# Optimization experiments

Measured on AMD Instinct MI355X. Metric: run time of the kernel, lower is better.

## Reference

```python
import jax, jax.numpy as jnp
import numpy as np

N_ROI = 116; G = 128; DEG = 32
N = G * N_ROI          # 14848 nodes
E = G * N_ROI * DEG    # 475136 edges
HID = 64; HEADS = 4; HC = HEADS * HID  # 256
EDIM = 5; EMB = 16; NG = 8; OUT = 2
NEG = 0.01      # nn.LeakyReLU default slope
NEG_ATT = 0.2   # GATv2 internal negative_slope
EPS = 1e-5


def leaky(x, s=NEG):
    return jnp.where(x >= 0, x, s * x)


def seg_softmax(logits, seg, n):
    # numerically stable softmax over edges grouped by target node
    m = jax.ops.segment_max(logits, seg, num_segments=n)
    m = jnp.where(jnp.isfinite(m), m, 0.0)
    ex = jnp.exp(logits - m[seg])
    s = jax.ops.segment_sum(ex, seg, num_segments=n)
    return ex / (s[seg] + 1e-16)


def _xav(k, shape):
    return jax.random.normal(k, shape, jnp.float32) * np.sqrt(2.0 / sum(shape)).astype(np.float32)


def setup_inputs() -> dict:
    key = jax.random.key(0)
    ks = jax.random.split(key, 40)
    x = jax.random.normal(ks[0], (N, N_ROI), jnp.float32)
    off = (jnp.arange(G, dtype=jnp.int32) * N_ROI)[:, None]
    src = (jax.random.randint(ks[1], (G, N_ROI * DEG), 0, N_ROI, jnp.int32) + off).reshape(-1)
    dst = (jax.random.randint(ks[2], (G, N_ROI * DEG), 0, N_ROI, jnp.int32) + off).reshape(-1)
    edge_index = jnp.stack([src, dst])  # [2, E], block-diagonal per graph
    edge_attr = jax.random.normal(ks[3], (E, EDIM), jnp.float32)
    grp = np.repeat(np.arange(NG, dtype=np.int32), [15] * 7 + [11])  # partition of 116 ROIs
    node_group = jnp.tile(jnp.asarray(grp), G)
    batch = jnp.repeat(jnp.arange(G, dtype=jnp.int32), N_ROI)
    p = {
        'group_emb': _xav(ks[4], (NG, EMB)),
        'W_embed': _xav(ks[5], (N_ROI + EMB, HID)), 'b_embed': jnp.zeros((HID,), jnp.float32),
        'We_enc': _xav(ks[6], (EDIM, HID)), 'be_enc': jnp.zeros((HID,), jnp.float32),
        'W1': _xav(ks[7], (HID, HID)), 'b1': jnp.zeros((HID,), jnp.float32),
        'W2': _xav(ks[8], (HID, HID)), 'b2': jnp.zeros((HID,), jnp.float32),
        'ln_g': jnp.ones((HID,), jnp.float32), 'ln_b': jnp.zeros((HID,), jnp.float32),
        'l0_Wl': _xav(ks[9], (HID, HC)), 'l0_Wr': _xav(ks[10], (HID, HC)),
        'l0_We': _xav(ks[11], (EDIM, HC)), 'l0_att': _xav(ks[12], (HEADS, HID)),
        'l0_b': jnp.zeros((HC,), jnp.float32),
        'l0_bn_g': jnp.ones((HC,), jnp.float32), 'l0_bn_b': jnp.zeros((HC,), jnp.float32),
        'l1_Wl': _xav(ks[13], (HC, HC)), 'l1_Wr': _xav(ks[14], (HC, HC)),
        'l1_We': _xav(ks[15], (EDIM, HC)), 'l1_att': _xav(ks[16], (HEADS, HID)),
        'l1_b': jnp.zeros((HC,), jnp.float32),
        'l1_bn_g': jnp.ones((HC,), jnp.float32), 'l1_bn_b': jnp.zeros((HC,), jnp.float32),
        'fc2_W': _xav(ks[17], (HC, OUT)), 'fc2_b': jnp.zeros((OUT,), jnp.float32),
    }
    return dict(x=x, edge_index=edge_index, edge_attr=edge_attr, batch=batch, node_group=node_group, **p)


def _gat_layer(h, src, dst, edge_attr, Wl, Wr, We, att, b, bn_g, bn_b):
    n = h.shape[0]
    xl = (h @ Wl).reshape(n, HEADS, HID)
    xr = (h @ Wr).reshape(n, HEADS, HID)
    e = (edge_attr @ We).reshape(-1, HEADS, HID)
    xls = xl[src]                                   # [E,H,C]
    z = leaky(xls + xr[dst] + e, NEG_ATT)
    logits = jnp.einsum('ehc,hc->eh', z, att)       # GATv2 attention scores
    alpha = seg_softmax(logits, dst, n)             # softmax over incoming edges per node
    out = jax.ops.segment_sum(xls * alpha[:, :, None], dst, num_segments=n)
    out = out.reshape(n, HC) + b
    mu = out.mean(0); var = ((out - mu) ** 2).mean(0)  # BatchNorm (batch stats)
    out = (out - mu) / jnp.sqrt(var + EPS) * bn_g + bn_b
    return leaky(out)


def reference(x, edge_index, edge_attr, batch, node_group, group_emb, W_embed, b_embed,
              We_enc, be_enc, W1, b1, W2, b2, ln_g, ln_b,
              l0_Wl, l0_Wr, l0_We, l0_att, l0_b, l0_bn_g, l0_bn_b,
              l1_Wl, l1_Wr, l1_We, l1_att, l1_b, l1_bn_g, l1_bn_b, fc2_W, fc2_b):
    src, dst = edge_index[0], edge_index[1]
    # BrainEncodeEmbed: group embedding concat + projection
    h = jnp.concatenate([x, group_emb[node_group]], axis=-1)   # [N, 132]
    h = leaky(h @ W_embed + b_embed)                            # [N, HID]
    eemb = leaky(edge_attr @ We_enc + be_enc)                   # [E, HID]
    # GINEConv: sum_j ReLU(x_j + e_ij), eps=0, then MLP
    msg = jax.nn.relu(h[src] + eemb)
    h = h + jax.ops.segment_sum(msg, dst, num_segments=N)
    h = leaky(h @ W1 + b1) @ W2 + b2
    h = leaky(h)
    mu = h.mean(-1, keepdims=True)
    v = ((h - mu) ** 2).mean(-1, keepdims=True)
    h = (h - mu) / jnp.sqrt(v + EPS) * ln_g + ln_b              # LayerNorm
    # stacked GATv2 blocks
    h = _gat_layer(h, src, dst, edge_attr, l0_Wl, l0_Wr, l0_We, l0_att, l0_b, l0_bn_g, l0_bn_b)
    h = _gat_layer(h, src, dst, edge_attr, l1_Wl, l1_Wr, l1_We, l1_att, l1_b, l1_bn_g, l1_bn_b)
    # global mean pool + classifier
    cnt = jax.ops.segment_sum(jnp.ones((h.shape[0],), h.dtype), batch, num_segments=G)
    pooled = jax.ops.segment_sum(h, batch, num_segments=G) / cnt[:, None]
    return pooled @ fc2_W + fc2_b
```

## Files before the change

### kernel.cpp

```cpp
#include <hip/hip_runtime.h>
#include <hip/hip_bf16.h>

#define NN     14848
#define NE     475136
#define NROI   116
#define NGRAPH 128
#define EPG    3712
#define HID    64
#define HC     256
#define NEG    0.01f
#define NEGA   0.2f
#define EPB    2304
#define XPAD   65

typedef __attribute__((ext_vector_type(8))) short short8;
typedef __attribute__((ext_vector_type(4))) float floatx4;

__device__ __forceinline__ float leaky(float x, float s) { return fmaxf(x, s * x); }

__device__ __forceinline__ short f2bf(float f) {
    unsigned u = __float_as_uint(f);
    unsigned r = (u + 0x7fffu + ((u >> 16) & 1u)) >> 16;
    return (short)r;
}

__global__ __launch_bounds__(256) void k_embed(
    const float* __restrict__ x, const int* __restrict__ ng,
    const float* __restrict__ gemb, const float* __restrict__ W,
    const float* __restrict__ b, float* __restrict__ h0)
{
    const int w = threadIdx.x >> 6, c = threadIdx.x & 63;
    const int n = blockIdx.x * 4 + w;
    __shared__ float in[4][132];
    for (int k = c; k < NROI; k += 64) in[w][k] = x[n * NROI + k];
    if (c < 16) in[w][NROI + c] = gemb[ng[n] * 16 + c];
    __syncthreads();
    float acc = b[c];
    #pragma unroll 4
    for (int k = 0; k < 132; k++) acc = fmaf(in[w][k], W[k * 64 + c], acc);
    h0[n * 64 + c] = leaky(acc, NEG);
}

__global__ __launch_bounds__(256) void k_csr(
    const int* __restrict__ src, const int* __restrict__ dst,
    const float* __restrict__ ea,
    int* __restrict__ row_start, int* __restrict__ row_cnt,
    int* __restrict__ ssd, float* __restrict__ ea_s)
{
    const int g = blockIdx.x, tid = threadIdx.x;
    const int e0 = g * EPG, nb = g * NROI;
    __shared__ int cnt[NROI], start[NROI], cur[NROI];
    if (tid < NROI) cnt[tid] = 0;
    __syncthreads();
    for (int i = tid; i < EPG; i += 256) atomicAdd(&cnt[dst[e0 + i] - nb], 1);
    __syncthreads();
    if (tid == 0) {
        int s = 0;
        for (int r = 0; r < NROI; r++) { start[r] = s; s += cnt[r]; }
    }
    __syncthreads();
    if (tid < NROI) {
        row_start[nb + tid] = e0 + start[tid];
        row_cnt[nb + tid] = cnt[tid];
        cur[tid] = start[tid];
    }
    __syncthreads();
    for (int i = tid; i < EPG; i += 256) {
        const int e = e0 + i, dl = dst[e] - nb;
        const int pos = atomicAdd(&cur[dl], 1);
        const int gi = e0 + pos;
        ssd[gi] = (src[e] - nb) | (dl << 16);
        const float4 q = make_float4(ea[e * 5], ea[e * 5 + 1], ea[e * 5 + 2], ea[e * 5 + 3]);
        *(float4*)&ea_s[(size_t)gi * 8] = q;
        ea_s[(size_t)gi * 8 + 4] = ea[e * 5 + 4];
    }
}

__global__ __launch_bounds__(64) void k_prep_w(
    const float* __restrict__ Wl0, const float* __restrict__ Wr0,
    const float* __restrict__ Wl1, const float* __restrict__ Wr1,
    short* __restrict__ Wt0, short* __restrict__ Wt1)
{
    if (blockIdx.x < 512) {
        const int n = blockIdx.x;
        for (int k = threadIdx.x; k < 64; k += 64) {
            const float v = (n < 256) ? Wl0[k * 256 + n] : Wr0[k * 256 + (n - 256)];
            Wt0[(size_t)n * 64 + k] = f2bf(v);
        }
    } else {
        const int n = blockIdx.x - 512;
        for (int k = threadIdx.x; k < 256; k += 64) {
            const float v = (n < 256) ? Wl1[k * 256 + n] : Wr1[k * 256 + (n - 256)];
            Wt1[(size_t)n * 256 + k] = f2bf(v);
        }
    }
}

__global__ __launch_bounds__(256) void k_gine_mlp_ln(
    const float* __restrict__ h0, const int* __restrict__ row_start,
    const int* __restrict__ row_cnt, const int* __restrict__ ssd,
    const float* __restrict__ ea_s,
    const float* __restrict__ We, const float* __restrict__ be,
    const float* __restrict__ W1, const float* __restrict__ b1,
    const float* __restrict__ W2, const float* __restrict__ b2,
    const float* __restrict__ lg_, const float* __restrict__ lb_,
    short* __restrict__ hn)
{
    const int tid = threadIdx.x, w = tid >> 6, lane = tid & 63;
    const int row = blockIdx.x * 4 + w;
    const int nb = (row / NROI) * NROI;
    const int st = row_start[row], cnt = row_cnt[row];
    const float w0 = We[lane], w1 = We[64 + lane], w2 = We[128 + lane],
                w3 = We[192 + lane], w4 = We[256 + lane];
    const float bec = be[lane];
    float g0 = 0.f, g1 = 0.f;
    int j = 0;
    for (; j + 2 <= cnt; j += 2) {
        const int ia = st + j, ib = st + j + 1;
        const int sa = nb + (ssd[ia] & 0xffff), sb = nb + (ssd[ib] & 0xffff);
        const float4 qa = *(const float4*)&ea_s[(size_t)ia * 8];
        const float qa4 = ea_s[(size_t)ia * 8 + 4];
        const float4 qb = *(const float4*)&ea_s[(size_t)ib * 8];
        const float qb4 = ea_s[(size_t)ib * 8 + 4];
        float ea_ = bec, eb_ = bec;
        ea_ = fmaf(qa.x, w0, ea_); eb_ = fmaf(qb.x, w0, eb_);
        ea_ = fmaf(qa.y, w1, ea_); eb_ = fmaf(qb.y, w1, eb_);
        ea_ = fmaf(qa.z, w2, ea_); eb_ = fmaf(qb.z, w2, eb_);
        ea_ = fmaf(qa.w, w3, ea_); eb_ = fmaf(qb.w, w3, eb_);
        ea_ = fmaf(qa4, w4, ea_);  eb_ = fmaf(qb4, w4, eb_);
        g0 += fmaxf(h0[sa * 64 + lane] + leaky(ea_, NEG), 0.f);
        g1 += fmaxf(h0[sb * 64 + lane] + leaky(eb_, NEG), 0.f);
    }
    for (; j < cnt; j++) {
        const int idx = st + j;
        const int s = nb + (ssd[idx] & 0xffff);
        const float4 q = *(const float4*)&ea_s[(size_t)idx * 8];
        const float q4 = ea_s[(size_t)idx * 8 + 4];
        float em = bec;
        em = fmaf(q.x, w0, em); em = fmaf(q.y, w1, em); em = fmaf(q.z, w2, em);
        em = fmaf(q.w, w3, em); em = fmaf(q4, w4, em);
        g0 += fmaxf(h0[s * 64 + lane] + leaky(em, NEG), 0.f);
    }
    const float aggv = g0 + g1;
    __shared__ float v[4][64], t[4][64];
    v[w][lane] = h0[row * 64 + lane] + aggv;
    __syncthreads();
    float a = b1[lane];
    #pragma unroll 8
    for (int k = 0; k < 64; k++) a = fmaf(v[w][k], W1[k * 64 + lane], a);
    t[w][lane] = leaky(a, NEG);
    __syncthreads();
    float o = b2[lane];
    #pragma unroll 8
    for (int k = 0; k < 64; k++) o = fmaf(t[w][k], W2[k * 64 + lane], o);
    o = leaky(o, NEG);
    float s = o;
    #pragma unroll
    for (int off = 32; off; off >>= 1) s += __shfl_xor(s, off);
    const float mu = s * (1.f / 64.f);
    const float d = o - mu;
    float s2 = d * d;
    #pragma unroll
    for (int off = 32; off; off >>= 1) s2 += __shfl_xor(s2, off);
    hn[row * 64 + lane] = f2bf(d * rsqrtf(s2 * (1.f / 64.f) + 1e-5f) * lg_[lane] + lb_[lane]);
}

__global__ __launch_bounds__(256) void k_bn_bf16(
    const float* __restrict__ V, const float* __restrict__ stats,
    const float* __restrict__ bg, const float* __restrict__ bb,
    short* __restrict__ Hb)
{
    const int n = blockIdx.x, c = threadIdx.x;
    const float inv_n = 1.f / (float)NN;
    const float mu = stats[c] * inv_n;
    float var = stats[256 + c] * inv_n - mu * mu;
    var = fmaxf(var, 0.f);
    const float rsg = rsqrtf(var + 1e-5f) * bg[c];
    const float o = (V[(size_t)n * HC + c] - mu) * rsg + bb[c];
    Hb[(size_t)n * HC + c] = f2bf(leaky(o, NEG));
}

template <int D>
__global__ __launch_bounds__(256) void k_gemm(
    const short* __restrict__ A, const short* __restrict__ Wt,
    float* __restrict__ X, float* __restrict__ Y)
{
    const int m0 = blockIdx.x * 16;
    const int w = threadIdx.x >> 6, lane = threadIdx.x & 63;
    const int n0 = w * 128;
    const int r = lane & 15, q = lane >> 4;
    floatx4 acc[8];
    #pragma unroll
    for (int t = 0; t < 8; t++) acc[t] = (floatx4){0.f, 0.f, 0.f, 0.f};
    const short* Arow = A + (size_t)(m0 + r) * D + q * 8;
    const short* Brow = Wt + (size_t)(n0 + r) * D + q * 8;
    #pragma unroll
    for (int k0 = 0; k0 < D; k0 += 32) {
        const short8 a = *(const short8*)(Arow + k0);
        #pragma unroll
        for (int t = 0; t < 8; t++) {
            const short8 b = *(const short8*)(Brow + (size_t)t * 16 * D + k0);
            acc[t] = __builtin_amdgcn_mfma_f32_16x16x32_bf16(a, b, acc[t], 0, 0, 0);
        }
    }
    #pragma unroll
    for (int t = 0; t < 8; t++) {
        const int ncol = n0 + t * 16 + r;
        #pragma unroll
        for (int g2 = 0; g2 < 4; g2++) {
            const int row = m0 + q * 4 + g2;
            if (ncol < 256) X[(size_t)row * HC + ncol] = acc[t][g2];
            else            Y[(size_t)row * HC + (ncol - 256)] = acc[t][g2];
        }
    }
}

__global__ __launch_bounds__(256, 4) void k_gat(
    const int* __restrict__ row_start, const int* __restrict__ row_cnt,
    const int* __restrict__ ssd, const float* __restrict__ ea_s,
    const float* __restrict__ We, const float* __restrict__ att,
    const float* __restrict__ bias,
    const float* __restrict__ X, const float* __restrict__ Y,
    float* __restrict__ V, float* __restrict__ stats)
{
    const int g = blockIdx.x >> 3;
    const int h = (blockIdx.x >> 1) & 3;
    const int half = blockIdx.x & 1;
    const int tid = threadIdx.x, w = tid >> 6, lane = tid & 63;
    const int nb = g * NROI, e0 = g * EPG, hc = h * 64;
    const int r0 = half * 58, r1 = r0 + 58;
    const int es = row_start[nb + r0];
    const int ee = (r1 < NROI) ? row_start[nb + r1] : e0 + EPG;

    __shared__ float Xs[NROI * XPAD];
    __shared__ float lg[EPB];
    __shared__ float inv_s[58];

    for (int r = w; r < NROI; r += 4)
        Xs[r * XPAD + lane] = X[(size_t)(nb + r) * HC + hc + lane];
    __syncthreads();

    const int ne = ee - es;
    for (int i = tid; i < ne; i += 256) {
        const int e = es + i;
        const int sd = ssd[e];
        const int sl = sd & 0xffff, dl = sd >> 16;
        const float4 q = *(const float4*)&ea_s[(size_t)e * 8];
        const float q4 = ea_s[(size_t)e * 8 + 4];
        const float* yrow = &Y[(size_t)(nb + dl) * HC + hc];
        const int xb = sl * XPAD;
        float lacc = 0.f;
        #pragma unroll 8
        for (int c = 0; c < 64; c++) {
            float ep = q.x * We[0 * HC + hc + c];
            ep = fmaf(q.y, We[1 * HC + hc + c], ep);
            ep = fmaf(q.z, We[2 * HC + hc + c], ep);
            ep = fmaf(q.w, We[3 * HC + hc + c], ep);
            ep = fmaf(q4, We[4 * HC + hc + c], ep);
            const float z = Xs[xb + c] + yrow[c] + ep;
            lacc = fmaf(att[hc + c], leaky(z, NEGA), lacc);
        }
        lg[i] = lacc;
    }
    __syncthreads();

    for (int r = r0 + w; r < r1; r += 4) {
        const int stl = row_start[nb + r] - es;
        const int cnt = row_cnt[nb + r];
        float m = -INFINITY;
        for (int j = lane; j < cnt; j += 64) m = fmaxf(m, lg[stl + j]);
        #pragma unroll
        for (int off = 32; off; off >>= 1) m = fmaxf(m, __shfl_xor(m, off));
        float s = 0.f;
        for (int j = lane; j < cnt; j += 64) {
            const float e_ = __expf(lg[stl + j] - m);
            lg[stl + j] = e_;
            s += e_;
        }
        #pragma unroll
        for (int off = 32; off; off >>= 1) s += __shfl_xor(s, off);
        if (lane == 0) inv_s[r - r0] = 1.f / (s + 1e-16f);
    }
    __syncthreads();

    float ps = 0.f, ps2 = 0.f;
    const float bb = bias[hc + lane];
    for (int r = r0 + w; r < r1; r += 4) {
        const int st = row_start[nb + r];
        const int cnt = row_cnt[nb + r];
        const int stl = st - es;
        float a0 = 0.f, a1 = 0.f, a2 = 0.f, a3 = 0.f;
        int j = 0;
        for (; j + 4 <= cnt; j += 4) {
            const int s0 = ssd[st + j] & 0xffff, s1 = ssd[st + j + 1] & 0xffff,
                      s2 = ssd[st + j + 2] & 0xffff, s3 = ssd[st + j + 3] & 0xffff;
            a0 = fmaf(Xs[s0 * XPAD + lane], lg[stl + j], a0);
            a1 = fmaf(Xs[s1 * XPAD + lane], lg[stl + j + 1], a1);
            a2 = fmaf(Xs[s2 * XPAD + lane], lg[stl + j + 2], a2);
            a3 = fmaf(Xs[s3 * XPAD + lane], lg[stl + j + 3], a3);
        }
        for (; j < cnt; j++)
            a0 = fmaf(Xs[(ssd[st + j] & 0xffff) * XPAD + lane], lg[stl + j], a0);
        const float vv = ((a0 + a1) + (a2 + a3)) * inv_s[r - r0] + bb;
        V[(size_t)(nb + r) * HC + hc + lane] = vv;
        ps += vv;
        ps2 += vv * vv;
    }
    __syncthreads();
    lg[tid] = ps;
    lg[256 + tid] = ps2;
    __syncthreads();
    if (tid < 64) {
        float s1 = 0.f, s2 = 0.f;
        #pragma unroll
        for (int w2 = 0; w2 < 4; w2++) {
            s1 += lg[w2 * 64 + tid];
            s2 += lg[256 + w2 * 64 + tid];
        }
        atomicAdd(&stats[hc + tid], s1);
        atomicAdd(&stats[256 + hc + tid], s2);
    }
}

__global__ __launch_bounds__(256) void k_pool_fc(
    const float* __restrict__ V, const float* __restrict__ stats,
    const float* __restrict__ bg, const float* __restrict__ bb,
    const float* __restrict__ fW, const float* __restrict__ fb,
    float* __restrict__ out)
{
    const int g = blockIdx.x, c = threadIdx.x;
    const float inv_n = 1.f / (float)NN;
    const float mu = stats[c] * inv_n;
    float var = stats[256 + c] * inv_n - mu * mu;
    var = fmaxf(var, 0.f);
    const float rsg = rsqrtf(var + 1e-5f) * bg[c];
    const float bbc = bb[c];
    float s = 0.f;
    for (int r = 0; r < NROI; r++) {
        const float vv = (V[(size_t)(g * NROI + r) * HC + c] - mu) * rsg + bbc;
        s += leaky(vv, NEG);
    }
    s *= (1.f / (float)NROI);
    __shared__ float red[256];
    for (int o = 0; o < 2; o++) {
        red[c] = s * fW[c * 2 + o];
        __syncthreads();
        for (int off = 128; off; off >>= 1) {
            if (c < off) red[c] += red[c + off];
            __syncthreads();
        }
        if (c == 0) out[g * 2 + o] = red[0] + fb[o];
        __syncthreads();
    }
}

extern "C" void kernel_launch(void* const* d_in, const int* in_sizes, int n_in,
                              void* d_out, int out_size, void* d_ws, size_t ws_size,
                              hipStream_t stream) {
    const float* x         = (const float*)d_in[0];
    const int*   edge_idx  = (const int*)d_in[1];
    const float* edge_attr = (const float*)d_in[2];
    const int*   node_grp  = (const int*)d_in[4];
    const float* group_emb = (const float*)d_in[5];
    const float* W_embed   = (const float*)d_in[6];
    const float* b_embed   = (const float*)d_in[7];
    const float* We_enc    = (const float*)d_in[8];
    const float* be_enc    = (const float*)d_in[9];
    const float* W1        = (const float*)d_in[10];
    const float* b1        = (const float*)d_in[11];
    const float* W2        = (const float*)d_in[12];
    const float* b2        = (const float*)d_in[13];
    const float* ln_g      = (const float*)d_in[14];
    const float* ln_b      = (const float*)d_in[15];
    const float* l0_Wl     = (const float*)d_in[16];
    const float* l0_Wr     = (const float*)d_in[17];
    const float* l0_We     = (const float*)d_in[18];
    const float* l0_att    = (const float*)d_in[19];
    const float* l0_b      = (const float*)d_in[20];
    const float* l0_bn_g   = (const float*)d_in[21];
    const float* l0_bn_b   = (const float*)d_in[22];
    const float* l1_Wl     = (const float*)d_in[23];
    const float* l1_Wr     = (const float*)d_in[24];
    const float* l1_We     = (const float*)d_in[25];
    const float* l1_att    = (const float*)d_in[26];
    const float* l1_b      = (const float*)d_in[27];
    const float* l1_bn_g   = (const float*)d_in[28];
    const float* l1_bn_b   = (const float*)d_in[29];
    const float* fc2_W     = (const float*)d_in[30];
    const float* fc2_b     = (const float*)d_in[31];

    const int* src = edge_idx;
    const int* dst = edge_idx + NE;

    float* ws     = (float*)d_ws;
    float* h0     = ws;
    float* X      = h0 + (size_t)64 * NN;
    float* Y      = X + (size_t)HC * NN;
    float* V      = Y + (size_t)HC * NN;
    float* stats0 = V + (size_t)HC * NN;
    float* stats1 = stats0 + 512;
    float* ea_s   = stats1 + 512;
    int* row_start = (int*)(ea_s + (size_t)8 * NE);
    int* row_cnt   = row_start + NN;
    int* ssd       = row_cnt + NN;
    short* hn_b    = (short*)(ssd + NE);
    short* Hb1     = hn_b + (size_t)64 * NN;
    short* Wt0     = Hb1 + (size_t)HC * NN;
    short* Wt1     = Wt0 + 512 * 64;

    float* out = (float*)d_out;

    hipMemsetAsync(stats0, 0, 1024 * sizeof(float), stream);
    k_embed<<<NN / 4, 256, 0, stream>>>(x, node_grp, group_emb, W_embed, b_embed, h0);
    k_csr<<<NGRAPH, 256, 0, stream>>>(src, dst, edge_attr, row_start, row_cnt, ssd, ea_s);
    k_prep_w<<<1024, 64, 0, stream>>>(l0_Wl, l0_Wr, l1_Wl, l1_Wr, Wt0, Wt1);
    k_gine_mlp_ln<<<NN / 4, 256, 0, stream>>>(h0, row_start, row_cnt, ssd, ea_s,
                                              We_enc, be_enc, W1, b1, W2, b2, ln_g, ln_b, hn_b);

    k_gemm<64><<<NN / 16, 256, 0, stream>>>(hn_b, Wt0, X, Y);
    k_gat<<<NGRAPH * 8, 256, 0, stream>>>(row_start, row_cnt, ssd, ea_s,
                                          l0_We, l0_att, l0_b, X, Y, V, stats0);

    k_bn_bf16<<<NN, 256, 0, stream>>>(V, stats0, l0_bn_g, l0_bn_b, Hb1);
    k_gemm<256><<<NN / 16, 256, 0, stream>>>(Hb1, Wt1, X, Y);
    k_gat<<<NGRAPH * 8, 256, 0, stream>>>(row_start, row_cnt, ssd, ea_s,
                                          l1_We, l1_att, l1_b, X, Y, V, stats1);

    k_pool_fc<<<NGRAPH, 256, 0, stream>>>(V, stats1, l1_bn_g, l1_bn_b, fc2_W, fc2_b, out);
}
```

Baseline: 454.1 us.

## Fuse BatchNorm+LeakyReLU into layer-1 GEMM, fold stats memset into CSR kernel

Removes the separate BatchNorm-to-bf16 kernel. The layer-1 GEMM now reads the fp32 V tensor directly and applies the per-channel scale/shift, LeakyReLU and bf16 conversion in registers, with the scale/shift precomputed into shared memory. The stats memset moves into the CSR kernel, saving one launch and one intermediate bf16 buffer round trip. The GAT logit loop also processes two channels per iteration with float2 loads and two accumulators. The GEMM now loads twice the A-operand bytes (fp32 instead of bf16) and does the redundant BN math once per column block.

```diff
diff --git a/kernel.cpp b/kernel.cpp
--- a/kernel.cpp
+++ b/kernel.cpp
@@ -45,9 +45,13 @@
     const int* __restrict__ src, const int* __restrict__ dst,
     const float* __restrict__ ea,
     int* __restrict__ row_start, int* __restrict__ row_cnt,
-    int* __restrict__ ssd, float* __restrict__ ea_s)
+    int* __restrict__ ssd, float* __restrict__ ea_s,
+    float* __restrict__ stats01)
 {
     const int g = blockIdx.x, tid = threadIdx.x;
+    if (g < 2) {
+        for (int i = tid; i < 512; i += 256) stats01[g * 512 + i] = 0.f;
+    }
     const int e0 = g * EPG, nb = g * NROI;
     __shared__ int cnt[NROI], start[NROI], cur[NROI];
     if (tid < NROI) cnt[tid] = 0;
@@ -165,38 +169,54 @@
     hn[row * 64 + lane] = f2bf(d * rsqrtf(s2 * (1.f / 64.f) + 1e-5f) * lg_[lane] + lb_[lane]);
 }
 
-__global__ __launch_bounds__(256) void k_bn_bf16(
-    const float* __restrict__ V, const float* __restrict__ stats,
-    const float* __restrict__ bg, const float* __restrict__ bb,
-    short* __restrict__ Hb)
-{
-    const int n = blockIdx.x, c = threadIdx.x;
-    const float inv_n = 1.f / (float)NN;
-    const float mu = stats[c] * inv_n;
-    float var = stats[256 + c] * inv_n - mu * mu;
-    var = fmaxf(var, 0.f);
-    const float rsg = rsqrtf(var + 1e-5f) * bg[c];
-    const float o = (V[(size_t)n * HC + c] - mu) * rsg + bb[c];
-    Hb[(size_t)n * HC + c] = f2bf(leaky(o, NEG));
-}
-
-template <int D>
+template <int D, bool BN>
 __global__ __launch_bounds__(256) void k_gemm(
-    const short* __restrict__ A, const short* __restrict__ Wt,
+    const short* __restrict__ A, const float* __restrict__ Vin,
+    const float* __restrict__ stats, const float* __restrict__ bn_g,
+    const float* __restrict__ bn_b,
+    const short* __restrict__ Wt,
     float* __restrict__ X, float* __restrict__ Y)
 {
     const int m0 = blockIdx.x * 16;
     const int w = threadIdx.x >> 6, lane = threadIdx.x & 63;
     const int n0 = w * 128;
     const int r = lane & 15, q = lane >> 4;
+    __shared__ float sc_s[256], sh_s[256];
+    if constexpr (BN) {
+        const int c = threadIdx.x;
+        const float inv_n = 1.f / (float)NN;
+        const float mu = stats[c] * inv_n;
+        float var = stats[256 + c] * inv_n - mu * mu;
+        var = fmaxf(var, 0.f);
+        const float rsg = rsqrtf(var + 1e-5f) * bn_g[c];
+        sc_s[c] = rsg;
+        sh_s[c] = bn_b[c] - mu * rsg;
+        __syncthreads();
+    }
     floatx4 acc[8];
     #pragma unroll
     for (int t = 0; t < 8; t++) acc[t] = (floatx4){0.f, 0.f, 0.f, 0.f};
     const short* Arow = A + (size_t)(m0 + r) * D + q * 8;
+    const float* Vrow = Vin + (size_t)(m0 + r) * D + q * 8;
     const short* Brow = Wt + (size_t)(n0 + r) * D + q * 8;
     #pragma unroll
     for (int k0 = 0; k0 < D; k0 += 32) {
-        const short8 a = *(const short8*)(Arow + k0);
+        short8 a;
+        if constexpr (BN) {
+            const float4 v0 = *(const float4*)(Vrow + k0);
+            const float4 v1 = *(const float4*)(Vrow + k0 + 4);
+            const int cb = q * 8 + k0;
+            a[0] = f2bf(leaky(fmaf(v0.x, sc_s[cb + 0], sh_s[cb + 0]), NEG));
+            a[1] = f2bf(leaky(fmaf(v0.y, sc_s[cb + 1], sh_s[cb + 1]), NEG));
+            a[2] = f2bf(leaky(fmaf(v0.z, sc_s[cb + 2], sh_s[cb + 2]), NEG));
+            a[3] = f2bf(leaky(fmaf(v0.w, sc_s[cb + 3], sh_s[cb + 3]), NEG));
+            a[4] = f2bf(leaky(fmaf(v1.x, sc_s[cb + 4], sh_s[cb + 4]), NEG));
+            a[5] = f2bf(leaky(fmaf(v1.y, sc_s[cb + 5], sh_s[cb + 5]), NEG));
+            a[6] = f2bf(leaky(fmaf(v1.z, sc_s[cb + 6], sh_s[cb + 6]), NEG));
+            a[7] = f2bf(leaky(fmaf(v1.w, sc_s[cb + 7], sh_s[cb + 7]), NEG));
+        } else {
+            a = *(const short8*)(Arow + k0);
+        }
         #pragma unroll
         for (int t = 0; t < 8; t++) {
             const short8 b = *(const short8*)(Brow + (size_t)t * 16 * D + k0);
@@ -249,18 +269,27 @@
         const float q4 = ea_s[(size_t)e * 8 + 4];
         const float* yrow = &Y[(size_t)(nb + dl) * HC + hc];
         const int xb = sl * XPAD;
-        float lacc = 0.f;
+        float l0 = 0.f, l1 = 0.f;
         #pragma unroll 8
-        for (int c = 0; c < 64; c++) {
-            float ep = q.x * We[0 * HC + hc + c];
-            ep = fmaf(q.y, We[1 * HC + hc + c], ep);
-            ep = fmaf(q.z, We[2 * HC + hc + c], ep);
-            ep = fmaf(q.w, We[3 * HC + hc + c], ep);
-            ep = fmaf(q4, We[4 * HC + hc + c], ep);
-            const float z = Xs[xb + c] + yrow[c] + ep;
-            lacc = fmaf(att[hc + c], leaky(z, NEGA), lacc);
-        }
-        lg[i] = lacc;
+        for (int c = 0; c < 64; c += 2) {
+            const float2 y2 = *(const float2*)(yrow + c);
+            const float xs0 = Xs[xb + c], xs1 = Xs[xb + c + 1];
+            float ep0 = q.x * We[0 * HC + hc + c];
+            ep0 = fmaf(q.y, We[1 * HC + hc + c], ep0);
+            ep0 = fmaf(q.z, We[2 * HC + hc + c], ep0);
+            ep0 = fmaf(q.w, We[3 * HC + hc + c], ep0);
+            ep0 = fmaf(q4, We[4 * HC + hc + c], ep0);
+            float ep1 = q.x * We[0 * HC + hc + c + 1];
+            ep1 = fmaf(q.y, We[1 * HC + hc + c + 1], ep1);
+            ep1 = fmaf(q.z, We[2 * HC + hc + c + 1], ep1);
+            ep1 = fmaf(q.w, We[3 * HC + hc + c + 1], ep1);
+            ep1 = fmaf(q4, We[4 * HC + hc + c + 1], ep1);
+            const float z0 = xs0 + y2.x + ep0;
+            const float z1 = xs1 + y2.y + ep1;
+            l0 = fmaf(att[hc + c], leaky(z0, NEGA), l0);
+            l1 = fmaf(att[hc + c + 1], leaky(z1, NEGA), l1);
+        }
+        lg[i] = l0 + l1;
     }
     __syncthreads();
 
@@ -404,25 +433,24 @@
     int* row_cnt   = row_start + NN;
     int* ssd       = row_cnt + NN;
     short* hn_b    = (short*)(ssd + NE);
-    short* Hb1     = hn_b + (size_t)64 * NN;
-    short* Wt0     = Hb1 + (size_t)HC * NN;
+    short* Wt0     = hn_b + (size_t)64 * NN;
     short* Wt1     = Wt0 + 512 * 64;
 
     float* out = (float*)d_out;
 
-    hipMemsetAsync(stats0, 0, 1024 * sizeof(float), stream);
     k_embed<<<NN / 4, 256, 0, stream>>>(x, node_grp, group_emb, W_embed, b_embed, h0);
-    k_csr<<<NGRAPH, 256, 0, stream>>>(src, dst, edge_attr, row_start, row_cnt, ssd, ea_s);
+    k_csr<<<NGRAPH, 256, 0, stream>>>(src, dst, edge_attr, row_start, row_cnt, ssd, ea_s, stats0);
     k_prep_w<<<1024, 64, 0, stream>>>(l0_Wl, l0_Wr, l1_Wl, l1_Wr, Wt0, Wt1);
     k_gine_mlp_ln<<<NN / 4, 256, 0, stream>>>(h0, row_start, row_cnt, ssd, ea_s,
                                               We_enc, be_enc, W1, b1, W2, b2, ln_g, ln_b, hn_b);
 
-    k_gemm<64><<<NN / 16, 256, 0, stream>>>(hn_b, Wt0, X, Y);
+    k_gemm<64, false><<<NN / 16, 256, 0, stream>>>(hn_b, nullptr, nullptr, nullptr, nullptr,
+                                                   Wt0, X, Y);
     k_gat<<<NGRAPH * 8, 256, 0, stream>>>(row_start, row_cnt, ssd, ea_s,
                                           l0_We, l0_att, l0_b, X, Y, V, stats0);
 
-    k_bn_bf16<<<NN, 256, 0, stream>>>(V, stats0, l0_bn_g, l0_bn_b, Hb1);
-    k_gemm<256><<<NN / 16, 256, 0, stream>>>(Hb1, Wt1, X, Y);
+    k_gemm<256, true><<<NN / 16, 256, 0, stream>>>(nullptr, V, stats0, l0_bn_g, l0_bn_b,
+                                                   Wt1, X, Y);
     k_gat<<<NGRAPH * 8, 256, 0, stream>>>(row_start, row_cnt, ssd, ea_s,
                                           l1_We, l1_att, l1_b, X, Y, V, stats1);
 
```

Result: no change. 451.9 us (-0.5%).
